# Kernel optimization log

Measured on AMD Instinct MI355X. Metric: run time of the kernel, lower is better.

Reference implementation:

```python
import jax, jax.numpy as jnp
import numpy as np

N_LEVELS = 1024
K = 8  # number of spike timesteps; d/T have length K+1 (index 0 unused)
X_SHAPE = (64, 512, 1024)


def setup_inputs() -> dict:
    key = jax.random.key(0)
    kx, kh0, kh, kd, kT = jax.random.split(key, 5)
    x = jax.random.normal(kx, X_SHAPE, dtype=jnp.float32) * 2.0
    # h: [N_LEVELS, K+1]; column 0 is the sorted search grid (required by searchsorted)
    h0 = jnp.sort(jax.random.uniform(kh0, (N_LEVELS,), minval=-4.0, maxval=4.0))
    h = jax.random.normal(kh, (N_LEVELS, K + 1), dtype=jnp.float32)
    h = h.at[:, 0].set(h0)
    d = jax.random.uniform(kd, (K + 1,), minval=0.05, maxval=1.0)
    T = jax.random.uniform(kT, (K + 1,), minval=-1.0, maxval=1.0)
    b = jnp.float32(0.1)
    return {"x": x, "h": h, "d": d, "T": T, "b": b}


def reference(x, h, d, T, b):
    sp = x.shape
    xf = x.reshape(-1)
    grid = h[:, 0]  # sorted lookup grid
    n = grid.shape[0]
    idx = jnp.clip(jnp.searchsorted(grid, xf), 1, n - 1)
    left = grid[idx - 1]
    right = grid[idx]
    take_left = jnp.abs(xf - left) < jnp.abs(xf - right)
    nearest = jnp.where(take_left, left, right)          # quantized input
    nidx = jnp.where(take_left, idx - 1, idx)            # per-element row into h
    kmax = d.shape[0] - 1
    v = nearest
    out = jnp.zeros_like(xf)
    # loop over the small fixed number of thresholds (data dims fully vectorized)
    for t in range(1, kmax + 1):
        z = (v - T[t] >= 0).astype(xf.dtype)
        out = out + z * d[t]
        if t != kmax:
            v = h[nidx, t + 1]  # irregular per-element gather
    out = out - b
    return out.reshape(sp)
```

## Files before the change

### kernel.cpp

```cpp
#include <hip/hip_runtime.h>
#include <math.h>

#define NL  1024
#define KP1 9
#define NB  8192

#define WS_TAB 4
#define WS_BS  1028
#define WS_BKT 2060

__device__ __forceinline__ unsigned oi(float f) {
    unsigned u = __float_as_uint(f);
    return (u & 0x80000000u) ? ~u : (u | 0x80000000u);
}
__device__ __forceinline__ float unoi(unsigned k) {
    return __uint_as_float((k & 0x80000000u) ? (k & 0x7fffffffu) : ~k);
}

__device__ __forceinline__ int bidx(float x, float lo0, float inv) {
    float t = (x - lo0) * inv;
    int j = (int)t;
    j = j < 0 ? 0 : j;
    j = j > (NB - 1) ? (NB - 1) : j;
    return j;
}

__global__ __launch_bounds__(1024) void build_kernel(
    const float* __restrict__ h, const float* __restrict__ d,
    const float* __restrict__ T, const float* __restrict__ bp,
    float* __restrict__ ws)
{
    __shared__ float s_g[NL];
    __shared__ float s_B[NL];
    __shared__ int   s_jb[NL];
    __shared__ float s_lo0, s_inv;

    const int tid = threadIdx.x;
    float g = h[tid * KP1];
    s_g[tid] = g;

    {
        float v = g, outv = 0.0f, b = bp[0];
#pragma unroll
        for (int t = 1; t <= 8; ++t) {
            float z = ((v - T[t]) >= 0.0f) ? 1.0f : 0.0f;
            outv = outv + z * d[t];
            if (t != 8) v = h[tid * KP1 + (t + 1)];
        }
        ws[WS_TAB + tid] = outv - b;
    }
    __syncthreads();

    if (tid < NL - 1) {
        float l = s_g[tid], r = s_g[tid + 1];
        unsigned a = oi(l), b2 = oi(r);
        while (a < b2) {
            unsigned m = a + ((b2 - a) >> 1);
            float xm = unoi(m);
            float dl = fabsf(xm - l), dr = fabsf(xm - r);
            if (!(dl < dr)) b2 = m; else a = m + 1;
        }
        s_B[tid] = unoi(a);
    } else {
        s_B[tid] = INFINITY;
    }
    __syncthreads();

    if (tid == 0) {
        float lo0 = s_B[0];
        float inv = (float)NB / (s_B[NL - 2] - lo0);
        s_lo0 = lo0; s_inv = inv;
        ws[0] = lo0; ws[1] = inv;
    }
    __syncthreads();

    float lo0 = s_lo0, inv = s_inv;
    s_jb[tid] = (tid < NL - 1) ? bidx(s_B[tid], lo0, inv) : 0x7fffffff;
    ws[WS_BS + tid] = s_B[tid];
    if (tid < 8) ws[WS_BS + NL + tid] = INFINITY;
    __syncthreads();

    unsigned short* bucket = (unsigned short*)(ws + WS_BKT);
    for (int j = tid; j < NB; j += 1024) {
        int lo = 0;
#pragma unroll
        for (int s = 512; s >= 1; s >>= 1)
            if (s_jb[lo + s - 1] < j) lo += s;
        bucket[j] = (unsigned short)lo;
    }
}

__global__ __launch_bounds__(256) void ps_act_kernel(
    const float* __restrict__ x,
    const float* __restrict__ ws,
    float* __restrict__ out,
    int n4)
{
    __shared__ float          stab[NL];
    __shared__ float          sBs[NL + 8];
    __shared__ unsigned short sbk[NB];

    const int tid = threadIdx.x;
    for (int i = tid; i < NL; i += 256)     stab[i] = ws[WS_TAB + i];
    for (int i = tid; i < NL + 8; i += 256) sBs[i]  = ws[WS_BS + i];
    const unsigned short* gbk = (const unsigned short*)(ws + WS_BKT);
    for (int i = tid; i < NB; i += 256)     sbk[i]  = gbk[i];
    const float lo0 = ws[0];
    const float inv = ws[1];
    __syncthreads();

    const float4* __restrict__ x4 = (const float4*)x;
    float4* __restrict__ o4 = (float4*)out;
    const int stride = gridDim.x * blockDim.x;

    for (int i4 = blockIdx.x * blockDim.x + tid; i4 < n4; i4 += stride) {
        float4 xv = x4[i4];
        float xin[4] = {xv.x, xv.y, xv.z, xv.w};
        float xo[4];
#pragma unroll
        for (int e = 0; e < 4; ++e) {
            float xf = xin[e];
            int j = bidx(xf, lo0, inv);
            int ni = sbk[j];
            while (sBs[ni] <= xf) ++ni;
            xo[e] = stab[ni];
        }
        o4[i4] = make_float4(xo[0], xo[1], xo[2], xo[3]);
    }
}

extern "C" void kernel_launch(void* const* d_in, const int* in_sizes, int n_in,
                              void* d_out, int out_size, void* d_ws, size_t ws_size,
                              hipStream_t stream) {
    const float* x = (const float*)d_in[0];
    const float* h = (const float*)d_in[1];
    const float* d = (const float*)d_in[2];
    const float* T = (const float*)d_in[3];
    const float* b = (const float*)d_in[4];
    float* out = (float*)d_out;
    float* ws  = (float*)d_ws;

    int n  = in_sizes[0];
    int n4 = n / 4;

    build_kernel<<<1, 1024, 0, stream>>>(h, d, T, b, ws);
    ps_act_kernel<<<4096, 256, 0, stream>>>(x, ws, out, n4);
}
```

Before: 255.6 us.

## Interleave boundary/value pairs, halve bucket table, vectorize LDS fill, nontemporal stores

Packs each decision boundary and its output value into one float2 in workspace and shared memory, so the linear probe reads both with a single LDS access instead of two separate arrays. Halves the bucket index table to 4096 entries, which shrinks the shared memory footprint and the per-block fill cost but can lengthen the linear scan per element. Shared memory fills now use 16-byte vector loads, and outputs are written with nontemporal stores to avoid polluting the cache.

```diff
diff --git a/kernel.cpp b/kernel.cpp
--- a/kernel.cpp
+++ b/kernel.cpp
@@ -3,11 +3,10 @@
 
 #define NL  1024
 #define KP1 9
-#define NB  8192
+#define NB  4096
 
-#define WS_TAB 4
-#define WS_BS  1028
-#define WS_BKT 2060
+#define WS_PAIR 4
+#define WS_BKT  (WS_PAIR + 2*(NL+8))
 
 __device__ __forceinline__ unsigned oi(float f) {
     unsigned u = __float_as_uint(f);
@@ -39,15 +38,16 @@
     float g = h[tid * KP1];
     s_g[tid] = g;
 
+    float outv;
     {
-        float v = g, outv = 0.0f, b = bp[0];
+        float v = g, o = 0.0f, b = bp[0];
 #pragma unroll
         for (int t = 1; t <= 8; ++t) {
             float z = ((v - T[t]) >= 0.0f) ? 1.0f : 0.0f;
-            outv = outv + z * d[t];
+            o = o + z * d[t];
             if (t != 8) v = h[tid * KP1 + (t + 1)];
         }
-        ws[WS_TAB + tid] = outv - b;
+        outv = o - b;
     }
     __syncthreads();
 
@@ -76,8 +76,13 @@
 
     float lo0 = s_lo0, inv = s_inv;
     s_jb[tid] = (tid < NL - 1) ? bidx(s_B[tid], lo0, inv) : 0x7fffffff;
-    ws[WS_BS + tid] = s_B[tid];
-    if (tid < 8) ws[WS_BS + NL + tid] = INFINITY;
+
+    ws[WS_PAIR + 2 * tid]     = s_B[tid];
+    ws[WS_PAIR + 2 * tid + 1] = outv;
+    if (tid < 8) {
+        ws[WS_PAIR + 2 * (NL + tid)]     = INFINITY;
+        ws[WS_PAIR + 2 * (NL + tid) + 1] = 0.0f;
+    }
     __syncthreads();
 
     unsigned short* bucket = (unsigned short*)(ws + WS_BKT);
@@ -90,27 +95,33 @@
     }
 }
 
+typedef float vf4 __attribute__((ext_vector_type(4)));
+
 __global__ __launch_bounds__(256) void ps_act_kernel(
     const float* __restrict__ x,
     const float* __restrict__ ws,
     float* __restrict__ out,
     int n4)
 {
-    __shared__ float          stab[NL];
-    __shared__ float          sBs[NL + 8];
-    __shared__ unsigned short sbk[NB];
+    __shared__ __align__(16) float          spair[2 * (NL + 8)];
+    __shared__ __align__(16) unsigned short sbk[NB];
 
     const int tid = threadIdx.x;
-    for (int i = tid; i < NL; i += 256)     stab[i] = ws[WS_TAB + i];
-    for (int i = tid; i < NL + 8; i += 256) sBs[i]  = ws[WS_BS + i];
-    const unsigned short* gbk = (const unsigned short*)(ws + WS_BKT);
-    for (int i = tid; i < NB; i += 256)     sbk[i]  = gbk[i];
+    {
+        const float4* wp4 = (const float4*)(ws + WS_PAIR);
+        float4* sp4 = (float4*)spair;
+        for (int i = tid; i < 2 * (NL + 8) / 4; i += 256) sp4[i] = wp4[i];
+        const uint4* wb4 = (const uint4*)(ws + WS_BKT);
+        uint4* sb4 = (uint4*)sbk;
+        for (int i = tid; i < NB * 2 / 16; i += 256) sb4[i] = wb4[i];
+    }
     const float lo0 = ws[0];
     const float inv = ws[1];
     __syncthreads();
 
     const float4* __restrict__ x4 = (const float4*)x;
     float4* __restrict__ o4 = (float4*)out;
+    const float2* pp = (const float2*)spair;
     const int stride = gridDim.x * blockDim.x;
 
     for (int i4 = blockIdx.x * blockDim.x + tid; i4 < n4; i4 += stride) {
@@ -122,10 +133,12 @@
             float xf = xin[e];
             int j = bidx(xf, lo0, inv);
             int ni = sbk[j];
-            while (sBs[ni] <= xf) ++ni;
-            xo[e] = stab[ni];
+            float2 pv = pp[ni];
+            while (pv.x <= xf) { ++ni; pv = pp[ni]; }
+            xo[e] = pv.y;
         }
-        o4[i4] = make_float4(xo[0], xo[1], xo[2], xo[3]);
+        vf4 ov = {xo[0], xo[1], xo[2], xo[3]};
+        __builtin_nontemporal_store(ov, (vf4*)&o4[i4]);
     }
 }
 
```

New measurement: 246.7 us. -3.5%, faster.
